# Kernel optimization log

Measured on AMD Instinct MI355X. Metric: run time of the kernel, lower is better.

Reference implementation:

```python
import jax, jax.numpy as jnp
import numpy as np

NEG_SLOPE = 0.01  # F.leaky_relu default
EPS = 1e-12       # F.normalize default eps

def _lrelu(h):
    return jnp.where(h > 0, h, NEG_SLOPE * h)

def setup_inputs() -> dict:
    key = jax.random.key(0)
    ks = jax.random.split(key, 16)
    N, E, D = 100000, 800000, 64
    x = jax.random.normal(ks[0], (N, D), dtype=jnp.float32)
    src = jax.random.randint(ks[1], (E,), 0, N, dtype=jnp.int32)
    dst = jax.random.randint(ks[2], (E,), 0, N, dtype=jnp.int32)
    def lin(k, fo, fi):
        k1, k2 = jax.random.split(k)
        s = 1.0 / np.sqrt(fi)
        w = jax.random.uniform(k1, (fo, fi), jnp.float32, -s, s)
        b = jax.random.uniform(k2, (fo,), jnp.float32, -s, s)
        return w, b
    w1, b1 = lin(ks[3], 256, D)
    w2, b2 = lin(ks[4], 128, 256)
    w3, b3 = lin(ks[5], 64, 128)
    w4, b4 = lin(ks[6], 1, 64)
    w_self, _ = lin(ks[7], D, D)   # SAGEConv fc_self (no bias)
    w_neigh, _ = lin(ks[8], D, D)  # SAGEConv fc_neigh (no bias)
    bias = jnp.zeros((D,), jnp.float32)  # SAGEConv bias param
    return dict(x=x, src=src, dst=dst, w1=w1, b1=b1, w2=w2, b2=b2,
                w3=w3, b3=b3, w4=w4, b4=b4,
                w_self=w_self, w_neigh=w_neigh, bias=bias)

def reference(x, src, dst, w1, b1, w2, b2, w3, b3, w4, b4, w_self, w_neigh, bias):
    N = x.shape[0]
    # per-edge score MLP on (h_u - h_v)
    d = x[src] - x[dst]                       # [E, D]
    h = _lrelu(d @ w1.T + b1)                 # [E, 256]
    h = _lrelu(h @ w2.T + b2)                 # [E, 128]
    h = _lrelu(h @ w3.T + b3)                 # [E, 64]
    e = jax.nn.sigmoid(h @ w4.T + b4)         # [E, 1]
    # SAGEConv 'mean' with edge weights: mean over incoming edges of e * x_src
    msg = e * x[src]                          # [E, D]
    s = jax.ops.segment_sum(msg, dst, num_segments=N)               # [N, D]
    deg = jax.ops.segment_sum(jnp.ones((src.shape[0],), x.dtype), dst,
                              num_segments=N)                        # [N]
    neigh = s / jnp.maximum(deg, 1.0)[:, None]
    A = x @ w_self.T + neigh @ w_neigh.T + bias
    A = _lrelu(A)
    norm = jnp.maximum(jnp.linalg.norm(A, axis=1, keepdims=True), EPS)
    A = A / norm
    return A, e
```

## Files before the change

kernel.cpp:

```cpp
#include <hip/hip_runtime.h>
#include <hip/hip_bf16.h>

typedef unsigned short u16;
typedef unsigned int   u32;
typedef __attribute__((ext_vector_type(8))) short short8;
typedef __attribute__((ext_vector_type(4))) float f32x4;

__device__ __forceinline__ u16 f2bf(float f) {
  u32 u = __float_as_uint(f);
  u += 0x7FFFu + ((u >> 16) & 1u);
  return (u16)(u >> 16);
}
__device__ __forceinline__ float bf2f(u16 h) { return __uint_as_float(((u32)h) << 16); }
__device__ __forceinline__ u32 pk2(float lo, float hi) {
  union { __hip_bfloat162 h; u32 u; } c;
  c.h = __float22bfloat162_rn(make_float2(lo, hi));
  return c.u;
}
__device__ __forceinline__ float lo16f(u32 u) { return __uint_as_float(u << 16); }
__device__ __forceinline__ float hi16f(u32 u) { return __uint_as_float(u & 0xffff0000u); }
__device__ __forceinline__ float lrelu(float v) { return v > 0.f ? v : 0.01f * v; }

__host__ __device__ __forceinline__ int sig(int c) {
  return ((c >> 5) << 5) | ((c & 12) << 1) | (((c >> 4) & 1) << 2) | (c & 3);
}

union U8 { u32 w[4]; short8 v; };

#define MFMA16(A, B, C) __builtin_amdgcn_mfma_f32_16x16x32_bf16(A, B, C, 0, 0, 0)

#define LDS_CHUNK8 5120
#define LDS_W3     4096


__global__ __launch_bounds__(512, 2) void edge_mlp(
    const float* __restrict__ x, const int* __restrict__ src, const int* __restrict__ dst,
    const short8* __restrict__ wcat,
    const float* __restrict__ b1p, const float* __restrict__ b2p, const float* __restrict__ b3p,
    const float* __restrict__ w4p, const float* __restrict__ b4,
    const int* __restrict__ rowptr, int* __restrict__ cursor,
    u16* __restrict__ msgbuf, float* __restrict__ eout, int E)
{
  __shared__ short8 ldsw[LDS_CHUNK8];
  const int tid  = threadIdx.x;
  const int lane = tid & 63;
  const int wv   = tid >> 6;
  const int g    = lane >> 4;
  const int r    = lane & 15;
  const int eb   = (blockIdx.x * 8 + wv) * 32;
  const int e0   = eb + r, e1 = eb + 16 + r;
  const int ec0  = e0 < E ? e0 : E - 1;
  const int ec1  = e1 < E ? e1 : E - 1;
  const int sn0 = src[ec0], dn0 = dst[ec0];
  const int sn1 = src[ec1], dn1 = dst[ec1];
  const float b4v = b4[0];

  const float* xsr0 = x + (size_t)sn0 * 64 + 8 * g;
  const float* xdr0 = x + (size_t)dn0 * 64 + 8 * g;
  const float* xsr1 = x + (size_t)sn1 * 64 + 8 * g;
  const float* xdr1 = x + (size_t)dn1 * 64 + 8 * g;
  const float4 a0s0 = *(const float4*)(xsr0),      a0s1 = *(const float4*)(xsr0 + 4);
  const float4 a0s2 = *(const float4*)(xsr0 + 32), a0s3 = *(const float4*)(xsr0 + 36);
  const float4 a0d0 = *(const float4*)(xdr0),      a0d1 = *(const float4*)(xdr0 + 4);
  const float4 a0d2 = *(const float4*)(xdr0 + 32), a0d3 = *(const float4*)(xdr0 + 36);
  const float4 a1s0 = *(const float4*)(xsr1),      a1s1 = *(const float4*)(xsr1 + 4);
  const float4 a1s2 = *(const float4*)(xsr1 + 32), a1s3 = *(const float4*)(xsr1 + 36);
  const float4 a1d0 = *(const float4*)(xdr1),      a1d1 = *(const float4*)(xdr1 + 4);
  const float4 a1d2 = *(const float4*)(xdr1 + 32), a1d3 = *(const float4*)(xdr1 + 36);

  short8 na0 = wcat[lane];
  short8 na1 = wcat[64 + lane];

  {
    const short8* gp = wcat + 2048 + wv * 64 + lane;
    short8*       lp = ldsw + wv * 64;
#pragma unroll
    for (int i = 0; i < 10; i++) {
      __builtin_amdgcn_global_load_lds(
          (const __attribute__((address_space(1))) u32*)(gp + i * 512),
          (__attribute__((address_space(3))) u32*)(lp + i * 512), 16, 0, 0);
    }
  }

  U8 bA0, bB0, bA1, bB1, sA0lo, sA0hi, sA1lo, sA1hi;
  bA0.w[0] = pk2(a0s0.x - a0d0.x, a0s0.y - a0d0.y);
  bA0.w[1] = pk2(a0s0.z - a0d0.z, a0s0.w - a0d0.w);
  bA0.w[2] = pk2(a0s1.x - a0d1.x, a0s1.y - a0d1.y);
  bA0.w[3] = pk2(a0s1.z - a0d1.z, a0s1.w - a0d1.w);
  bB0.w[0] = pk2(a0s2.x - a0d2.x, a0s2.y - a0d2.y);
  bB0.w[1] = pk2(a0s2.z - a0d2.z, a0s2.w - a0d2.w);
  bB0.w[2] = pk2(a0s3.x - a0d3.x, a0s3.y - a0d3.y);
  bB0.w[3] = pk2(a0s3.z - a0d3.z, a0s3.w - a0d3.w);
  bA1.w[0] = pk2(a1s0.x - a1d0.x, a1s0.y - a1d0.y);
  bA1.w[1] = pk2(a1s0.z - a1d0.z, a1s0.w - a1d0.w);
  bA1.w[2] = pk2(a1s1.x - a1d1.x, a1s1.y - a1d1.y);
  bA1.w[3] = pk2(a1s1.z - a1d1.z, a1s1.w - a1d1.w);
  bB1.w[0] = pk2(a1s2.x - a1d2.x, a1s2.y - a1d2.y);
  bB1.w[1] = pk2(a1s2.z - a1d2.z, a1s2.w - a1d2.w);
  bB1.w[2] = pk2(a1s3.x - a1d3.x, a1s3.y - a1d3.y);
  bB1.w[3] = pk2(a1s3.z - a1d3.z, a1s3.w - a1d3.w);
  sA0lo.w[0] = pk2(a0s0.x, a0s0.y); sA0lo.w[1] = pk2(a0s0.z, a0s0.w);
  sA0lo.w[2] = pk2(a0s1.x, a0s1.y); sA0lo.w[3] = pk2(a0s1.z, a0s1.w);
  sA0hi.w[0] = pk2(a0s2.x, a0s2.y); sA0hi.w[1] = pk2(a0s2.z, a0s2.w);
  sA0hi.w[2] = pk2(a0s3.x, a0s3.y); sA0hi.w[3] = pk2(a0s3.z, a0s3.w);
  sA1lo.w[0] = pk2(a1s0.x, a1s0.y); sA1lo.w[1] = pk2(a1s0.z, a1s0.w);
  sA1lo.w[2] = pk2(a1s1.x, a1s1.y); sA1lo.w[3] = pk2(a1s1.z, a1s1.w);
  sA1hi.w[0] = pk2(a1s2.x, a1s2.y); sA1hi.w[1] = pk2(a1s2.z, a1s2.w);
  sA1hi.w[2] = pk2(a1s3.x, a1s3.y); sA1hi.w[3] = pk2(a1s3.z, a1s3.w);

  u32 h1a[32], h1b[32];
  {
    const float* b1l = b1p + 4 * g;
#pragma unroll
    for (int t = 0; t < 16; t++) {
      short8 a0 = na0, a1 = na1;
      if (t < 15) {
        na0 = wcat[(2 * t + 2) * 64 + lane];
        na1 = wcat[(2 * t + 3) * 64 + lane];
      }
      f32x4 p = {}, q = {};
      p = MFMA16(a0, bA0.v, p); p = MFMA16(a1, bB0.v, p);
      q = MFMA16(a0, bA1.v, q); q = MFMA16(a1, bB1.v, q);
      float4 bb = *(const float4*)(b1l + 16 * t);
      h1a[2 * t]     = pk2(lrelu(p[0] + bb.x), lrelu(p[1] + bb.y));
      h1a[2 * t + 1] = pk2(lrelu(p[2] + bb.z), lrelu(p[3] + bb.w));
      h1b[2 * t]     = pk2(lrelu(q[0] + bb.x), lrelu(q[1] + bb.y));
      h1b[2 * t + 1] = pk2(lrelu(q[2] + bb.z), lrelu(q[3] + bb.w));
    }
  }
  __syncthreads();

  u32 h2a[16], h2b[16];
  {
    const float* b2l = b2p + 4 * g;
#pragma unroll
    for (int t = 0; t < 8; t++) {
      f32x4 p = {}, q = {};
#pragma unroll
      for (int s = 0; s < 8; s++) {
        short8 a = ldsw[(t * 8 + s) * 64 + lane];
        U8 f0, f1;
        f0.w[0] = h1a[4 * s + 0]; f0.w[1] = h1a[4 * s + 1];
        f0.w[2] = h1a[4 * s + 2]; f0.w[3] = h1a[4 * s + 3];
        f1.w[0] = h1b[4 * s + 0]; f1.w[1] = h1b[4 * s + 1];
        f1.w[2] = h1b[4 * s + 2]; f1.w[3] = h1b[4 * s + 3];
        p = MFMA16(a, f0.v, p);
        q = MFMA16(a, f1.v, q);
      }
      float4 bb = *(const float4*)(b2l + 16 * t);
      h2a[2 * t]     = pk2(lrelu(p[0] + bb.x), lrelu(p[1] + bb.y));
      h2a[2 * t + 1] = pk2(lrelu(p[2] + bb.z), lrelu(p[3] + bb.w));
      h2b[2 * t]     = pk2(lrelu(q[0] + bb.x), lrelu(q[1] + bb.y));
      h2b[2 * t + 1] = pk2(lrelu(q[2] + bb.z), lrelu(q[3] + bb.w));
    }
  }

  float dot0 = 0.f, dot1 = 0.f;
  {
    const float* b3l = b3p + 4 * g;
    const float* w4l = w4p + 4 * g;
#pragma unroll
    for (int t = 0; t < 4; t++) {
      f32x4 p = {}, q = {};
#pragma unroll
      for (int s = 0; s < 4; s++) {
        short8 a = ldsw[LDS_W3 + (t * 4 + s) * 64 + lane];
        U8 f0, f1;
        f0.w[0] = h2a[4 * s + 0]; f0.w[1] = h2a[4 * s + 1];
        f0.w[2] = h2a[4 * s + 2]; f0.w[3] = h2a[4 * s + 3];
        f1.w[0] = h2b[4 * s + 0]; f1.w[1] = h2b[4 * s + 1];
        f1.w[2] = h2b[4 * s + 2]; f1.w[3] = h2b[4 * s + 3];
        p = MFMA16(a, f0.v, p);
        q = MFMA16(a, f1.v, q);
      }
      float4 bb = *(const float4*)(b3l + 16 * t);
      float4 ww = *(const float4*)(w4l + 16 * t);
      dot0 += lrelu(p[0] + bb.x) * ww.x + lrelu(p[1] + bb.y) * ww.y
            + lrelu(p[2] + bb.z) * ww.z + lrelu(p[3] + bb.w) * ww.w;
      dot1 += lrelu(q[0] + bb.x) * ww.x + lrelu(q[1] + bb.y) * ww.y
            + lrelu(q[2] + bb.z) * ww.z + lrelu(q[3] + bb.w) * ww.w;
    }
  }
  dot0 += __shfl_xor(dot0, 16); dot0 += __shfl_xor(dot0, 32);
  dot1 += __shfl_xor(dot1, 16); dot1 += __shfl_xor(dot1, 32);
  const float ev0 = 1.f / (1.f + __expf(-(dot0 + b4v)));
  const float ev1 = 1.f / (1.f + __expf(-(dot1 + b4v)));

  int pos0 = 0, pos1 = 0;
  if (g == 0) {
    if (e0 < E) { eout[e0] = ev0; pos0 = rowptr[dn0] + atomicAdd(&cursor[dn0], 1); }
    if (e1 < E) { eout[e1] = ev1; pos1 = rowptr[dn1] + atomicAdd(&cursor[dn1], 1); }
  }
  pos0 = __shfl(pos0, r);
  pos1 = __shfl(pos1, r);
  if (e0 < E) {
    u16* mp = msgbuf + (size_t)pos0 * 64 + g * 16;
    U8 m;
    m.w[0] = pk2(ev0 * lo16f(sA0lo.w[0]), ev0 * hi16f(sA0lo.w[0]));
    m.w[1] = pk2(ev0 * lo16f(sA0lo.w[1]), ev0 * hi16f(sA0lo.w[1]));
    m.w[2] = pk2(ev0 * lo16f(sA0lo.w[2]), ev0 * hi16f(sA0lo.w[2]));
    m.w[3] = pk2(ev0 * lo16f(sA0lo.w[3]), ev0 * hi16f(sA0lo.w[3]));
    *(short8*)(mp) = m.v;
    m.w[0] = pk2(ev0 * lo16f(sA0hi.w[0]), ev0 * hi16f(sA0hi.w[0]));
    m.w[1] = pk2(ev0 * lo16f(sA0hi.w[1]), ev0 * hi16f(sA0hi.w[1]));
    m.w[2] = pk2(ev0 * lo16f(sA0hi.w[2]), ev0 * hi16f(sA0hi.w[2]));
    m.w[3] = pk2(ev0 * lo16f(sA0hi.w[3]), ev0 * hi16f(sA0hi.w[3]));
    *(short8*)(mp + 8) = m.v;
  }
  if (e1 < E) {
    u16* mp = msgbuf + (size_t)pos1 * 64 + g * 16;
    U8 m;
    m.w[0] = pk2(ev1 * lo16f(sA1lo.w[0]), ev1 * hi16f(sA1lo.w[0]));
    m.w[1] = pk2(ev1 * lo16f(sA1lo.w[1]), ev1 * hi16f(sA1lo.w[1]));
    m.w[2] = pk2(ev1 * lo16f(sA1lo.w[2]), ev1 * hi16f(sA1lo.w[2]));
    m.w[3] = pk2(ev1 * lo16f(sA1lo.w[3]), ev1 * hi16f(sA1lo.w[3]));
    *(short8*)(mp) = m.v;
    m.w[0] = pk2(ev1 * lo16f(sA1hi.w[0]), ev1 * hi16f(sA1hi.w[0]));
    m.w[1] = pk2(ev1 * lo16f(sA1hi.w[1]), ev1 * hi16f(sA1hi.w[1]));
    m.w[2] = pk2(ev1 * lo16f(sA1hi.w[2]), ev1 * hi16f(sA1hi.w[2]));
    m.w[3] = pk2(ev1 * lo16f(sA1hi.w[3]), ev1 * hi16f(sA1hi.w[3]));
    *(short8*)(mp + 8) = m.v;
  }
}

__global__ void deg_hist(const int* __restrict__ dst, int* __restrict__ degi, int E)
{
  const int i = blockIdx.x * 256 + threadIdx.x;
  if (i < E) atomicAdd(&degi[dst[i]], 1);
}

__global__ void scan_part(const int* __restrict__ degi, int* __restrict__ rowptr,
                          int* __restrict__ bsum, int N)
{
  __shared__ int wsum[4];
  const int tid = threadIdx.x, lane = tid & 63, w = tid >> 6;
  const int base = blockIdx.x * 1024 + tid * 4;
  int d0 = 0, d1 = 0, d2 = 0, d3 = 0;
  if (base + 3 < N) {
    int4 v = *(const int4*)(degi + base);
    d0 = v.x; d1 = v.y; d2 = v.z; d3 = v.w;
  } else {
    if (base < N)     d0 = degi[base];
    if (base + 1 < N) d1 = degi[base + 1];
    if (base + 2 < N) d2 = degi[base + 2];
    if (base + 3 < N) d3 = degi[base + 3];
  }
  const int ts = d0 + d1 + d2 + d3;
  int sc = ts;
#pragma unroll
  for (int o = 1; o < 64; o <<= 1) { int v = __shfl_up(sc, o); if (lane >= o) sc += v; }
  if (lane == 63) wsum[w] = sc;
  __syncthreads();
  int woff = 0;
  for (int i = 0; i < w; i++) woff += wsum[i];
  const int ex = woff + sc - ts;
  if (base < N)     rowptr[base]     = ex;
  if (base + 1 < N) rowptr[base + 1] = ex + d0;
  if (base + 2 < N) rowptr[base + 2] = ex + d0 + d1;
  if (base + 3 < N) rowptr[base + 3] = ex + d0 + d1 + d2;
  if (tid == 255) bsum[blockIdx.x] = woff + sc;
}

__global__ void scan_bsum(int* __restrict__ bsum, int nb)
{
  __shared__ int wsum[4];
  const int tid = threadIdx.x, lane = tid & 63, w = tid >> 6;
  const int v = tid < nb ? bsum[tid] : 0;
  int sc = v;
#pragma unroll
  for (int o = 1; o < 64; o <<= 1) { int t = __shfl_up(sc, o); if (lane >= o) sc += t; }
  if (lane == 63) wsum[w] = sc;
  __syncthreads();
  int woff = 0;
  for (int i = 0; i < w; i++) woff += wsum[i];
  if (tid < nb) bsum[tid] = woff + sc - v;
}

__global__ void scan_add(int* __restrict__ rowptr, const int* __restrict__ bsum,
                         int* __restrict__ cursor, int N, int E)
{
  const int base = blockIdx.x * 1024 + threadIdx.x * 4;
  const int off = bsum[blockIdx.x];
#pragma unroll
  for (int i = 0; i < 4; i++)
    if (base + i < N) { rowptr[base + i] += off; cursor[base + i] = 0; }
  if (blockIdx.x == 0 && threadIdx.x == 0) rowptr[N] = E;
}

__global__ __launch_bounds__(256, 4) void node_agg_mfma(
    const float* __restrict__ x, const u16* __restrict__ msgbuf,
    const int* __restrict__ rowptr, const short8* __restrict__ wfin,
    const float* __restrict__ bias, float* __restrict__ A, int N)
{
  __shared__ short8 ldsW[1024];
  __shared__ float  nbuf[4][16][68];
  const int tid = threadIdx.x, wv = tid >> 6, lane = tid & 63;
  const int g = lane >> 4, r = lane & 15;
  for (int i = tid; i < 1024; i += 256) ldsW[i] = wfin[i];

  const int n0 = (blockIdx.x * 4 + wv) * 16;
  const int nr = (n0 + r) < N ? (n0 + r) : N - 1;
  const float* xp = x + (size_t)nr * 64 + 8 * g;
  const float4 xf0 = *(const float4*)(xp);
  const float4 xf1 = *(const float4*)(xp + 4);
  const float4 xf2 = *(const float4*)(xp + 32);
  const float4 xf3 = *(const float4*)(xp + 36);
  int rp = 0;
  if (lane < 17) rp = rowptr[min(n0 + lane, N)];
  const int cch = (((lane >> 3) & 1) << 5) | ((lane >> 4) << 3) | (lane & 7);
  for (int rr = 0; rr < 16; rr++) {
    const int s = __shfl(rp, rr);
    const int t = __shfl(rp, rr + 1);
    float acc = 0.f;
    for (int j = s; j < t; j += 4) {
      const int j1 = (j + 1 < t) ? j + 1 : j;
      const int j2 = (j + 2 < t) ? j + 2 : j;
      const int j3 = (j + 3 < t) ? j + 3 : j;
      const float v0 = bf2f(msgbuf[(size_t)j  * 64 + lane]);
      const float v1 = bf2f(msgbuf[(size_t)j1 * 64 + lane]);
      const float v2 = bf2f(msgbuf[(size_t)j2 * 64 + lane]);
      const float v3 = bf2f(msgbuf[(size_t)j3 * 64 + lane]);
      const float m1 = (j + 1 < t) ? 1.f : 0.f;
      const float m2 = (j + 2 < t) ? 1.f : 0.f;
      const float m3 = (j + 3 < t) ? 1.f : 0.f;
      acc += v0 + m1 * v1 + m2 * v2 + m3 * v3;
    }
    const float inv = 1.f / fmaxf((float)(t - s), 1.f);
    nbuf[wv][rr][cch] = acc * inv;
  }
  __syncthreads();

  U8 bf0, bf1, bf2q, bf3q;
  bf0.w[0] = pk2(xf0.x, xf0.y); bf0.w[1] = pk2(xf0.z, xf0.w);
  bf0.w[2] = pk2(xf1.x, xf1.y); bf0.w[3] = pk2(xf1.z, xf1.w);
  bf1.w[0] = pk2(xf2.x, xf2.y); bf1.w[1] = pk2(xf2.z, xf2.w);
  bf1.w[2] = pk2(xf3.x, xf3.y); bf1.w[3] = pk2(xf3.z, xf3.w);
  {
    const float* nb = nbuf[wv][r];
    const float4 n0v = *(const float4*)(nb + 8 * g);
    const float4 n1v = *(const float4*)(nb + 8 * g + 4);
    const float4 n2v = *(const float4*)(nb + 32 + 8 * g);
    const float4 n3v = *(const float4*)(nb + 32 + 8 * g + 4);
    bf2q.w[0] = pk2(n0v.x, n0v.y); bf2q.w[1] = pk2(n0v.z, n0v.w);
    bf2q.w[2] = pk2(n1v.x, n1v.y); bf2q.w[3] = pk2(n1v.z, n1v.w);
    bf3q.w[0] = pk2(n2v.x, n2v.y); bf3q.w[1] = pk2(n2v.z, n2v.w);
    bf3q.w[2] = pk2(n3v.x, n3v.y); bf3q.w[3] = pk2(n3v.z, n3v.w);
  }

  f32x4 acct[4] = {};
#pragma unroll
  for (int t = 0; t < 4; t++) {
    acct[t] = MFMA16(ldsW[(t * 4 + 0) * 64 + lane], bf0.v,  acct[t]);
    acct[t] = MFMA16(ldsW[(t * 4 + 1) * 64 + lane], bf1.v,  acct[t]);
    acct[t] = MFMA16(ldsW[(t * 4 + 2) * 64 + lane], bf2q.v, acct[t]);
    acct[t] = MFMA16(ldsW[(t * 4 + 3) * 64 + lane], bf3q.v, acct[t]);
  }

  f32x4 av[4];
  float ss = 0.f;
#pragma unroll
  for (int t = 0; t < 4; t++) {
    const float4 bb = *(const float4*)(bias + 16 * t + 4 * g);
    av[t][0] = lrelu(acct[t][0] + bb.x);
    av[t][1] = lrelu(acct[t][1] + bb.y);
    av[t][2] = lrelu(acct[t][2] + bb.z);
    av[t][3] = lrelu(acct[t][3] + bb.w);
    ss += av[t][0] * av[t][0] + av[t][1] * av[t][1]
        + av[t][2] * av[t][2] + av[t][3] * av[t][3];
  }
  ss += __shfl_xor(ss, 16); ss += __shfl_xor(ss, 32);
  const float rn = 1.f / fmaxf(sqrtf(ss), 1e-12f);
  if (n0 + r < N) {
    float* ap = A + (size_t)(n0 + r) * 64 + 4 * g;
#pragma unroll
    for (int t = 0; t < 4; t++) {
      float4 o;
      o.x = av[t][0] * rn; o.y = av[t][1] * rn;
      o.z = av[t][2] * rn; o.w = av[t][3] * rn;
      *(float4*)(ap + 16 * t) = o;
    }
  }
}

__global__ void convert_w(const float* __restrict__ w1, const float* __restrict__ w2,
                          const float* __restrict__ w3,
                          const float* __restrict__ b1, const float* __restrict__ b2,
                          const float* __restrict__ b3, const float* __restrict__ w4,
                          const float* __restrict__ w_self, const float* __restrict__ w_neigh,
                          u16* __restrict__ wcat, u16* __restrict__ wfin,
                          float* __restrict__ b1p, float* __restrict__ b2p,
                          float* __restrict__ b3p, float* __restrict__ w4p)
{
  const int idx = blockIdx.x * 256 + threadIdx.x;
  if (idx < 57344) {
    const float* w; int K, nsteps, loc;
    if (idx < 16384)      { loc = idx;         w = w1; K = 64;  nsteps = 2; }
    else if (idx < 49152) { loc = idx - 16384; w = w2; K = 256; nsteps = 8; }
    else                  { loc = idx - 49152; w = w3; K = 128; nsteps = 4; }
    const int chunk = loc >> 9;
    const int lane  = (loc >> 3) & 63;
    const int j     = loc & 7;
    const int t = chunk / nsteps, s = chunk % nsteps;
    const int m = sig(t * 16 + (lane & 15));
    const int k = s * 32 + (lane >> 4) * 8 + j;
    wcat[idx] = f2bf(w[m * K + k]);
  } else if (idx < 65536) {
    const int o = idx - 57344;
    const int c = o >> 9, lane = (o >> 3) & 63, j = o & 7;
    const int t = c >> 2, s = c & 3;
    const int m = 16 * t + (lane & 15);
    const int k = 32 * s + ((lane >> 4) << 3) + j;
    wfin[o] = f2bf(k < 64 ? w_self[m * 64 + k] : w_neigh[m * 64 + (k - 64)]);
  }
  if (idx < 256) b1p[idx] = b1[sig(idx)];
  if (idx < 128) b2p[idx] = b2[sig(idx)];
  if (idx < 64)  { b3p[idx] = b3[sig(idx)]; w4p[idx] = w4[sig(idx)]; }
}

extern "C" void kernel_launch(void* const* d_in, const int* in_sizes, int n_in,
                              void* d_out, int out_size, void* d_ws, size_t ws_size,
                              hipStream_t stream)
{
  const float* x       = (const float*)d_in[0];
  const int*   src     = (const int*)d_in[1];
  const int*   dst     = (const int*)d_in[2];
  const float* w1      = (const float*)d_in[3];
  const float* b1      = (const float*)d_in[4];
  const float* w2      = (const float*)d_in[5];
  const float* b2      = (const float*)d_in[6];
  const float* w3      = (const float*)d_in[7];
  const float* b3      = (const float*)d_in[8];
  const float* w4      = (const float*)d_in[9];
  const float* b4      = (const float*)d_in[10];
  const float* w_self  = (const float*)d_in[11];
  const float* w_neigh = (const float*)d_in[12];
  const float* bias    = (const float*)d_in[13];

  const int N = in_sizes[0] / 64;
  const int E = in_sizes[1];

  float* A    = (float*)d_out;
  float* eout = (float*)d_out + (size_t)N * 64;

  char* ws = (char*)d_ws;
  size_t off = 0;
  auto alloc = [&](size_t bytes) {
    void* p = ws + off;
    off = (off + bytes + 255) & ~(size_t)255;
    return p;
  };
  int*    degi   = (int*)alloc((size_t)N * 4);
  int*    rowptr = (int*)alloc((size_t)(N + 1) * 4);
  int*    cursor = (int*)alloc((size_t)N * 4);
  int*    bsum   = (int*)alloc(1024 * 4);
  short8* wcat   = (short8*)alloc((size_t)57344 * 2);
  short8* wfin   = (short8*)alloc((size_t)8192 * 2);
  float*  b1p    = (float*)alloc(256 * 4);
  float*  b2p    = (float*)alloc(128 * 4);
  float*  b3p    = (float*)alloc(64 * 4);
  float*  w4p    = (float*)alloc(64 * 4);
  u16*    msgbuf = (u16*)alloc((size_t)E * 128);

  hipMemsetAsync(degi, 0, (size_t)N * sizeof(int), stream);

  convert_w<<<256, 256, 0, stream>>>(w1, w2, w3, b1, b2, b3, w4, w_self, w_neigh,
                                     (u16*)wcat, (u16*)wfin, b1p, b2p, b3p, w4p);

  deg_hist<<<(E + 255) / 256, 256, 0, stream>>>(dst, degi, E);

  const int nsb = (N + 1023) / 1024;
  scan_part<<<nsb, 256, 0, stream>>>(degi, rowptr, bsum, N);
  scan_bsum<<<1, 256, 0, stream>>>(bsum, nsb);
  scan_add<<<nsb, 256, 0, stream>>>(rowptr, bsum, cursor, N, E);

  const int nblk = (E + 255) / 256;
  edge_mlp<<<nblk, 512, 0, stream>>>(x, src, dst, wcat, b1p, b2p, b3p, w4p, b4,
                                     rowptr, cursor, msgbuf, eout, E);

  const int nblk2 = (N + 63) / 64;
  node_agg_mfma<<<nblk2, 256, 0, stream>>>(x, msgbuf, rowptr, wfin, bias, A, N);
}
```

Baseline: 334.5 us.

## Precompute per-edge CSR slot in histogram, stage all MLP weights in LDS

The degree histogram now records each edge's atomic return value as its in-row order, so edge_mlp computes its CSR slot as rowptr[dst]+ord and no longer needs a second atomic pass or a cursor reset. W1 is also staged into LDS together with W2/W3, using 14 async chunks instead of 10, and the block barrier moves up front. Register arrays are also repacked as short8 unions to avoid per-iteration repacking. This adds an E-sized ord buffer and raises LDS use to 112KB per block, which may limit occupancy below the launch bound of 2 blocks.

```diff
diff --git a/kernel.cpp b/kernel.cpp
--- a/kernel.cpp
+++ b/kernel.cpp
@@ -29,8 +29,9 @@
 
 #define MFMA16(A, B, C) __builtin_amdgcn_mfma_f32_16x16x32_bf16(A, B, C, 0, 0, 0)
 
-#define LDS_CHUNK8 5120
-#define LDS_W3     4096
+#define W2_BASE 2048
+#define W3_BASE 6144
+#define NCHUNK8 7168
 
 
 __global__ __launch_bounds__(512, 2) void edge_mlp(
@@ -38,10 +39,10 @@
     const short8* __restrict__ wcat,
     const float* __restrict__ b1p, const float* __restrict__ b2p, const float* __restrict__ b3p,
     const float* __restrict__ w4p, const float* __restrict__ b4,
-    const int* __restrict__ rowptr, int* __restrict__ cursor,
+    const int* __restrict__ rowptr, const int* __restrict__ ord,
     u16* __restrict__ msgbuf, float* __restrict__ eout, int E)
 {
-  __shared__ short8 ldsw[LDS_CHUNK8];
+  __shared__ short8 ldsw[NCHUNK8];
   const int tid  = threadIdx.x;
   const int lane = tid & 63;
   const int wv   = tid >> 6;
@@ -67,20 +68,20 @@
   const float4 a1s2 = *(const float4*)(xsr1 + 32), a1s3 = *(const float4*)(xsr1 + 36);
   const float4 a1d0 = *(const float4*)(xdr1),      a1d1 = *(const float4*)(xdr1 + 4);
   const float4 a1d2 = *(const float4*)(xdr1 + 32), a1d3 = *(const float4*)(xdr1 + 36);
-
-  short8 na0 = wcat[lane];
-  short8 na1 = wcat[64 + lane];
+  const int pos0 = rowptr[dn0] + ord[ec0];
+  const int pos1 = rowptr[dn1] + ord[ec1];
 
   {
-    const short8* gp = wcat + 2048 + wv * 64 + lane;
+    const short8* gp = wcat + wv * 64 + lane;
     short8*       lp = ldsw + wv * 64;
 #pragma unroll
-    for (int i = 0; i < 10; i++) {
+    for (int i = 0; i < 14; i++) {
       __builtin_amdgcn_global_load_lds(
           (const __attribute__((address_space(1))) u32*)(gp + i * 512),
           (__attribute__((address_space(3))) u32*)(lp + i * 512), 16, 0, 0);
     }
   }
+  __syncthreads();
 
   U8 bA0, bB0, bA1, bB1, sA0lo, sA0hi, sA1lo, sA1hi;
   bA0.w[0] = pk2(a0s0.x - a0d0.x, a0s0.y - a0d0.y);
@@ -108,29 +109,26 @@
   sA1hi.w[0] = pk2(a1s2.x, a1s2.y); sA1hi.w[1] = pk2(a1s2.z, a1s2.w);
   sA1hi.w[2] = pk2(a1s3.x, a1s3.y); sA1hi.w[3] = pk2(a1s3.z, a1s3.w);
 
-  u32 h1a[32], h1b[32];
+  U8 h1A[8], h1B[8];
   {
     const float* b1l = b1p + 4 * g;
 #pragma unroll
     for (int t = 0; t < 16; t++) {
-      short8 a0 = na0, a1 = na1;
-      if (t < 15) {
-        na0 = wcat[(2 * t + 2) * 64 + lane];
-        na1 = wcat[(2 * t + 3) * 64 + lane];
-      }
+      short8 a0 = ldsw[(t * 2 + 0) * 64 + lane];
+      short8 a1 = ldsw[(t * 2 + 1) * 64 + lane];
       f32x4 p = {}, q = {};
       p = MFMA16(a0, bA0.v, p); p = MFMA16(a1, bB0.v, p);
       q = MFMA16(a0, bA1.v, q); q = MFMA16(a1, bB1.v, q);
       float4 bb = *(const float4*)(b1l + 16 * t);
-      h1a[2 * t]     = pk2(lrelu(p[0] + bb.x), lrelu(p[1] + bb.y));
-      h1a[2 * t + 1] = pk2(lrelu(p[2] + bb.z), lrelu(p[3] + bb.w));
-      h1b[2 * t]     = pk2(lrelu(q[0] + bb.x), lrelu(q[1] + bb.y));
-      h1b[2 * t + 1] = pk2(lrelu(q[2] + bb.z), lrelu(q[3] + bb.w));
-    }
-  }
-  __syncthreads();
-
-  u32 h2a[16], h2b[16];
+      const int w0 = 2 * t, w1 = 2 * t + 1;
+      h1A[w0 >> 2].w[w0 & 3] = pk2(lrelu(p[0] + bb.x), lrelu(p[1] + bb.y));
+      h1A[w1 >> 2].w[w1 & 3] = pk2(lrelu(p[2] + bb.z), lrelu(p[3] + bb.w));
+      h1B[w0 >> 2].w[w0 & 3] = pk2(lrelu(q[0] + bb.x), lrelu(q[1] + bb.y));
+      h1B[w1 >> 2].w[w1 & 3] = pk2(lrelu(q[2] + bb.z), lrelu(q[3] + bb.w));
+    }
+  }
+
+  U8 h2A[4], h2B[4];
   {
     const float* b2l = b2p + 4 * g;
 #pragma unroll
@@ -138,20 +136,16 @@
       f32x4 p = {}, q = {};
 #pragma unroll
       for (int s = 0; s < 8; s++) {
-        short8 a = ldsw[(t * 8 + s) * 64 + lane];
-        U8 f0, f1;
-        f0.w[0] = h1a[4 * s + 0]; f0.w[1] = h1a[4 * s + 1];
-        f0.w[2] = h1a[4 * s + 2]; f0.w[3] = h1a[4 * s + 3];
-        f1.w[0] = h1b[4 * s + 0]; f1.w[1] = h1b[4 * s + 1];
-        f1.w[2] = h1b[4 * s + 2]; f1.w[3] = h1b[4 * s + 3];
-        p = MFMA16(a, f0.v, p);
-        q = MFMA16(a, f1.v, q);
+        short8 a = ldsw[W2_BASE + (t * 8 + s) * 64 + lane];
+        p = MFMA16(a, h1A[s].v, p);
+        q = MFMA16(a, h1B[s].v, q);
       }
       float4 bb = *(const float4*)(b2l + 16 * t);
-      h2a[2 * t]     = pk2(lrelu(p[0] + bb.x), lrelu(p[1] + bb.y));
-      h2a[2 * t + 1] = pk2(lrelu(p[2] + bb.z), lrelu(p[3] + bb.w));
-      h2b[2 * t]     = pk2(lrelu(q[0] + bb.x), lrelu(q[1] + bb.y));
-      h2b[2 * t + 1] = pk2(lrelu(q[2] + bb.z), lrelu(q[3] + bb.w));
+      const int w0 = 2 * t, w1 = 2 * t + 1;
+      h2A[w0 >> 2].w[w0 & 3] = pk2(lrelu(p[0] + bb.x), lrelu(p[1] + bb.y));
+      h2A[w1 >> 2].w[w1 & 3] = pk2(lrelu(p[2] + bb.z), lrelu(p[3] + bb.w));
+      h2B[w0 >> 2].w[w0 & 3] = pk2(lrelu(q[0] + bb.x), lrelu(q[1] + bb.y));
+      h2B[w1 >> 2].w[w1 & 3] = pk2(lrelu(q[2] + bb.z), lrelu(q[3] + bb.w));
     }
   }
 
@@ -164,14 +158,9 @@
       f32x4 p = {}, q = {};
 #pragma unroll
       for (int s = 0; s < 4; s++) {
-        short8 a = ldsw[LDS_W3 + (t * 4 + s) * 64 + lane];
-        U8 f0, f1;
-        f0.w[0] = h2a[4 * s + 0]; f0.w[1] = h2a[4 * s + 1];
-        f0.w[2] = h2a[4 * s + 2]; f0.w[3] = h2a[4 * s + 3];
-        f1.w[0] = h2b[4 * s + 0]; f1.w[1] = h2b[4 * s + 1];
-        f1.w[2] = h2b[4 * s + 2]; f1.w[3] = h2b[4 * s + 3];
-        p = MFMA16(a, f0.v, p);
-        q = MFMA16(a, f1.v, q);
+        short8 a = ldsw[W3_BASE + (t * 4 + s) * 64 + lane];
+        p = MFMA16(a, h2A[s].v, p);
+        q = MFMA16(a, h2B[s].v, q);
       }
       float4 bb = *(const float4*)(b3l + 16 * t);
       float4 ww = *(const float4*)(w4l + 16 * t);
@@ -186,13 +175,10 @@
   const float ev0 = 1.f / (1.f + __expf(-(dot0 + b4v)));
   const float ev1 = 1.f / (1.f + __expf(-(dot1 + b4v)));
 
-  int pos0 = 0, pos1 = 0;
   if (g == 0) {
-    if (e0 < E) { eout[e0] = ev0; pos0 = rowptr[dn0] + atomicAdd(&cursor[dn0], 1); }
-    if (e1 < E) { eout[e1] = ev1; pos1 = rowptr[dn1] + atomicAdd(&cursor[dn1], 1); }
-  }
-  pos0 = __shfl(pos0, r);
-  pos1 = __shfl(pos1, r);
+    if (e0 < E) eout[e0] = ev0;
+    if (e1 < E) eout[e1] = ev1;
+  }
   if (e0 < E) {
     u16* mp = msgbuf + (size_t)pos0 * 64 + g * 16;
     U8 m;
@@ -223,10 +209,11 @@
   }
 }
 
-__global__ void deg_hist(const int* __restrict__ dst, int* __restrict__ degi, int E)
+__global__ void deg_hist(const int* __restrict__ dst, int* __restrict__ degi,
+                         int* __restrict__ ord, int E)
 {
   const int i = blockIdx.x * 256 + threadIdx.x;
-  if (i < E) atomicAdd(&degi[dst[i]], 1);
+  if (i < E) ord[i] = atomicAdd(&degi[dst[i]], 1);
 }
 
 __global__ void scan_part(const int* __restrict__ degi, int* __restrict__ rowptr,
@@ -277,13 +264,13 @@
 }
 
 __global__ void scan_add(int* __restrict__ rowptr, const int* __restrict__ bsum,
-                         int* __restrict__ cursor, int N, int E)
+                         int N, int E)
 {
   const int base = blockIdx.x * 1024 + threadIdx.x * 4;
   const int off = bsum[blockIdx.x];
 #pragma unroll
   for (int i = 0; i < 4; i++)
-    if (base + i < N) { rowptr[base + i] += off; cursor[base + i] = 0; }
+    if (base + i < N) rowptr[base + i] += off;
   if (blockIdx.x == 0 && threadIdx.x == 0) rowptr[N] = E;
 }
 
@@ -451,7 +438,7 @@
   };
   int*    degi   = (int*)alloc((size_t)N * 4);
   int*    rowptr = (int*)alloc((size_t)(N + 1) * 4);
-  int*    cursor = (int*)alloc((size_t)N * 4);
+  int*    ord    = (int*)alloc((size_t)E * 4);
   int*    bsum   = (int*)alloc(1024 * 4);
   short8* wcat   = (short8*)alloc((size_t)57344 * 2);
   short8* wfin   = (short8*)alloc((size_t)8192 * 2);
@@ -466,16 +453,16 @@
   convert_w<<<256, 256, 0, stream>>>(w1, w2, w3, b1, b2, b3, w4, w_self, w_neigh,
                                      (u16*)wcat, (u16*)wfin, b1p, b2p, b3p, w4p);
 
-  deg_hist<<<(E + 255) / 256, 256, 0, stream>>>(dst, degi, E);
+  deg_hist<<<(E + 255) / 256, 256, 0, stream>>>(dst, degi, ord, E);
 
   const int nsb = (N + 1023) / 1024;
   scan_part<<<nsb, 256, 0, stream>>>(degi, rowptr, bsum, N);
   scan_bsum<<<1, 256, 0, stream>>>(bsum, nsb);
-  scan_add<<<nsb, 256, 0, stream>>>(rowptr, bsum, cursor, N, E);
+  scan_add<<<nsb, 256, 0, stream>>>(rowptr, bsum, N, E);
 
   const int nblk = (E + 255) / 256;
   edge_mlp<<<nblk, 512, 0, stream>>>(x, src, dst, wcat, b1p, b2p, b3p, w4p, b4,
-                                     rowptr, cursor, msgbuf, eout, E);
+                                     rowptr, ord, msgbuf, eout, E);
 
   const int nblk2 = (N + 63) / 64;
   node_agg_mfma<<<nblk2, 256, 0, stream>>>(x, msgbuf, rowptr, wfin, bias, A, N);
```

After: 296.7 us. -11.3%, faster.
